# Kernel tuning notes

Measured on AMD Instinct MI355X. Metric: run time of the kernel, lower is better.

The kernel has to match this reference:

```python
import jax, jax.numpy as jnp
import numpy as np
from jax import lax

B, D_IN, LOW_DIM, NUM_CLASS, MOCO_QUEUE = 4096, 1024, 128, 32, 65536
PROTO_M, MOCO_M, EPS = 0.99, 0.999, 1e-12


def l2norm(x, axis=-1):
    n = jnp.linalg.norm(x, axis=axis, keepdims=True)
    return x / jnp.maximum(n, EPS)


def encoder(x, W_cls, b_cls, W_proj):
    # base_encoder returns (class logits, l2-normalized low-dim embedding)
    return x @ W_cls + b_cls, l2norm(x @ W_proj)


def setup_inputs() -> dict:
    key = jax.random.key(0)
    k = jax.random.split(key, 12)
    img_q = jax.random.normal(k[0], (B, D_IN), jnp.float32)
    im_k = jax.random.normal(k[1], (B, D_IN), jnp.float32)
    true_lab = jax.random.randint(k[2], (B,), 0, NUM_CLASS)
    partial_Y = (jax.random.uniform(k[3], (B, NUM_CLASS)) < 0.3).astype(jnp.float32)
    partial_Y = partial_Y.at[jnp.arange(B), true_lab].set(1.0)  # guarantee nonempty candidate set
    W_cls_q = 0.02 * jax.random.normal(k[4], (D_IN, NUM_CLASS), jnp.float32)
    b_cls_q = jnp.zeros((NUM_CLASS,), jnp.float32)
    W_proj_q = 0.02 * jax.random.normal(k[5], (D_IN, LOW_DIM), jnp.float32)
    # key encoder initialized near query encoder (copied then momentum-drifted)
    W_cls_k = W_cls_q + 0.002 * jax.random.normal(k[6], (D_IN, NUM_CLASS), jnp.float32)
    b_cls_k = jnp.zeros((NUM_CLASS,), jnp.float32)
    W_proj_k = W_proj_q + 0.002 * jax.random.normal(k[7], (D_IN, LOW_DIM), jnp.float32)
    queue = jax.random.normal(k[8], (MOCO_QUEUE, LOW_DIM), jnp.float32)
    queue = queue / jnp.maximum(jnp.linalg.norm(queue, axis=0, keepdims=True), EPS)  # F.normalize(queue, dim=0) as in __init__
    queue_pseudo = jax.random.normal(k[9], (MOCO_QUEUE, NUM_CLASS), jnp.float32)
    queue_partial = jax.random.normal(k[10], (MOCO_QUEUE, NUM_CLASS), jnp.float32)
    prototypes = l2norm(jax.random.normal(k[11], (NUM_CLASS, LOW_DIM), jnp.float32))
    return dict(img_q=img_q, im_k=im_k, partial_Y=partial_Y,
                W_cls_q=W_cls_q, b_cls_q=b_cls_q, W_proj_q=W_proj_q,
                W_cls_k=W_cls_k, b_cls_k=b_cls_k, W_proj_k=W_proj_k,
                prototypes=prototypes, queue=queue,
                queue_pseudo=queue_pseudo, queue_partial=queue_partial)


def reference(img_q, im_k, partial_Y, W_cls_q, b_cls_q, W_proj_q,
              W_cls_k, b_cls_k, W_proj_k, prototypes, queue,
              queue_pseudo, queue_partial):
    output, q = encoder(img_q, W_cls_q, b_cls_q, W_proj_q)
    predicted_scores = jax.nn.softmax(output, axis=1) * partial_Y
    pseudo_labels = jnp.argmax(predicted_scores, axis=1)  # (B,) int
    # prototypes are detached before the similarity (clone().detach())
    score_prot = jax.nn.softmax(q @ lax.stop_gradient(prototypes).T, axis=1)
    # order-dependent per-sample EMA scatter (faithful to the python for-loop,
    # including within-batch label collisions) -> lax.scan recurrence
    qd = lax.stop_gradient(q)
    def step(p, xs):
        feat, lab = xs
        return p.at[lab].set(p[lab] * PROTO_M + (1.0 - PROTO_M) * feat), None
    new_protos, _ = lax.scan(step, lax.stop_gradient(prototypes), (qd, pseudo_labels))
    new_protos = l2norm(new_protos)
    # momentum key-encoder update (no grad), then key features
    Wck = lax.stop_gradient(W_cls_k * MOCO_M + W_cls_q * (1.0 - MOCO_M))
    bck = lax.stop_gradient(b_cls_k * MOCO_M + b_cls_q * (1.0 - MOCO_M))
    Wpk = lax.stop_gradient(W_proj_k * MOCO_M + W_proj_q * (1.0 - MOCO_M))
    _, kfeat = encoder(im_k, Wck, bck, Wpk)
    kfeat = lax.stop_gradient(kfeat)
    qv = lax.stop_gradient(queue)
    qp = lax.stop_gradient(queue_pseudo)
    qpt = lax.stop_gradient(queue_partial)
    features = jnp.concatenate([q, kfeat, qv], axis=0)
    pseudo_scores = jnp.concatenate([predicted_scores, predicted_scores, qp], axis=0)
    partial_target = jnp.concatenate([partial_Y, partial_Y, qpt], axis=0)
    # dequeue-and-enqueue at ptr=0 (buffer state update, no grad)
    new_queue = qv.at[0:B].set(kfeat)
    new_queue_pseudo = qp.at[0:B].set(lax.stop_gradient(predicted_scores))
    new_queue_partial = qpt.at[0:B].set(lax.stop_gradient(partial_Y))
    return (output, features, pseudo_scores, partial_target, score_prot,
            new_protos, new_queue, new_queue_pseudo, new_queue_partial)
```

## Files before the change

### kernel.cpp

```cpp
#include <hip/hip_runtime.h>
#include <hip/hip_bf16.h>
#include <stdint.h>


typedef __attribute__((ext_vector_type(8))) short bf16x8;
typedef __attribute__((ext_vector_type(4))) float f32x4;

constexpr size_t O0 = 0;
constexpr size_t O1 = 131072;
constexpr size_t O2 = 9568256;
constexpr size_t O3 = 11927552;
constexpr size_t O4 = 14286848;
constexpr size_t O5 = 14417920;
constexpr size_t O6 = 14422016;
constexpr size_t O7 = 22810624;
constexpr size_t O8 = 24907776;

__device__ __forceinline__ unsigned short f2b(float x) {
  union { float f; uint32_t u; } v; v.f = x;
  uint32_t u = v.u;
  uint32_t r = (u + 0x7fffu + ((u >> 16) & 1u)) >> 16;
  return (unsigned short)r;
}

#define SWZ(r, cb) ((((r) * 128) + (cb)) ^ (((r) & 7) << 4))

__global__ __launch_bounds__(256) void prep(
    const float* __restrict__ Wpq, const float* __restrict__ Wcq,
    const float* __restrict__ Wpk,
    unsigned short* __restrict__ wt_q, unsigned short* __restrict__ wt_pk) {
  const int bid = blockIdx.x;
  const int t = threadIdx.x;
  const float *W1, *W2 = nullptr;
  float a1 = 1.f, a2 = 0.f;
  unsigned short* dst;
  int kb, nbr, nbw, N;
  if (bid < 128) {
    W1 = Wpq; N = 128; kb = (bid & 31) * 32; nbr = nbw = (bid >> 5) * 32;
    dst = wt_q;
  } else if (bid < 160) {
    W1 = Wcq; N = 32; kb = (bid - 128) * 32; nbr = 0; nbw = 128; dst = wt_q;
  } else {
    W1 = Wpk; W2 = Wpq; a1 = 0.999f; a2 = 0.001f; N = 128;
    const int b = bid - 160; kb = (b & 31) * 32; nbr = nbw = (b >> 5) * 32;
    dst = wt_pk;
  }
  __shared__ float tile[32][33];
  const int tx = t & 31, ty = t >> 5;
#pragma unroll
  for (int j = 0; j < 4; ++j) {
    const int k = kb + ty + 8 * j;
    float v = W1[(size_t)k * N + nbr + tx] * a1;
    if (W2) v += W2[(size_t)k * N + nbr + tx] * a2;
    tile[ty + 8 * j][tx] = v;
  }
  __syncthreads();
#pragma unroll
  for (int j = 0; j < 4; ++j) {
    const int n = nbw + ty + 8 * j;
    dst[(size_t)n * 1024 + kb + tx] = f2b(tile[tx][ty + 8 * j]);
  }
}

__global__ __launch_bounds__(320) void gemm_fused(
    const float* __restrict__ img_q, const float* __restrict__ im_k,
    const unsigned short* __restrict__ wt_q,
    const unsigned short* __restrict__ wt_pk,
    const float* __restrict__ bias, const float* __restrict__ partialY,
    const float* __restrict__ protos, float* __restrict__ out,
    int* __restrict__ labels) {
  __shared__ __align__(16) unsigned char smem[28672];
  unsigned char* sA = smem;
  unsigned char* sB = smem + 2048;
  const int bid = blockIdx.x;
  const int t = threadIdx.x;
  const int w = t >> 6, l = t & 63;
  const int ar = l & 15, kg = l >> 4;
  const bool isq = bid < 256;
  const int m0 = (isq ? bid : bid - 256) * 16;
  const float* A = isq ? img_q : im_k;
  const unsigned short* Wt = isq ? wt_q : wt_pk;
  const int BROWS8 = isq ? 1280 : 1024;
  const int arow = t >> 4, acol = t & 15;

  float4 avA, avB;
  uint4 bvA[4], bvB[4];
  if (t < 256) {
    avA = *(const float4*)(A + (size_t)(m0 + arow) * 1024 + acol * 4);
    avB = *(const float4*)(A + (size_t)(m0 + arow) * 1024 + 64 + acol * 4);
  }
#pragma unroll
  for (int i = 0; i < 4; ++i) {
    const int cid = t + i * 320;
    if (cid < BROWS8) {
      const int r = cid >> 3, c = cid & 7;
      bvA[i] = *(const uint4*)(Wt + (size_t)r * 1024 + c * 8);
      bvB[i] = *(const uint4*)(Wt + (size_t)r * 1024 + 64 + c * 8);
    }
  }
  f32x4 acc0 = {0.f, 0.f, 0.f, 0.f}, acc1 = {0.f, 0.f, 0.f, 0.f};

#define STAGE(av, bv)                                                        \
  {                                                                          \
    if (t < 256) {                                                           \
      uint2 pk;                                                              \
      pk.x = (uint32_t)f2b(av.x) | ((uint32_t)f2b(av.y) << 16);              \
      pk.y = (uint32_t)f2b(av.z) | ((uint32_t)f2b(av.w) << 16);              \
      *(uint2*)(sA + SWZ(arow, acol * 8)) = pk;                              \
    }                                                                        \
    _Pragma("unroll") for (int i = 0; i < 4; ++i) {                          \
      const int cid = t + i * 320;                                           \
      if (cid < BROWS8) {                                                    \
        const int r = cid >> 3, c = cid & 7;                                 \
        *(uint4*)(sB + SWZ(r, c * 16)) = bv[i];                              \
      }                                                                      \
    }                                                                        \
  }
#define RELOAD(av, bv, kt)                                                   \
  {                                                                          \
    const int k0 = (kt) * 64;                                                \
    if (t < 256)                                                             \
      av = *(const float4*)(A + (size_t)(m0 + arow) * 1024 + k0 + acol * 4); \
    _Pragma("unroll") for (int i = 0; i < 4; ++i) {                          \
      const int cid = t + i * 320;                                           \
      if (cid < BROWS8) {                                                    \
        const int r = cid >> 3, c = cid & 7;                                 \
        bv[i] = *(const uint4*)(Wt + (size_t)r * 1024 + k0 + c * 8);         \
      }                                                                      \
    }                                                                        \
  }
#define MFMA_PHASE()                                                         \
  if (isq || w < 4) {                                                        \
    _Pragma("unroll") for (int s = 0; s < 2; ++s) {                          \
      const int ch = (s * 4 + kg) * 16;                                      \
      bf16x8 a = *(const bf16x8*)(sA + SWZ(ar, ch));                         \
      const int r0 = w * 32 + ar, r1 = w * 32 + 16 + ar;                     \
      bf16x8 b0 = *(const bf16x8*)(sB + SWZ(r0, ch));                        \
      bf16x8 b1 = *(const bf16x8*)(sB + SWZ(r1, ch));                        \
      acc0 = __builtin_amdgcn_mfma_f32_16x16x32_bf16(a, b0, acc0, 0, 0, 0);  \
      acc1 = __builtin_amdgcn_mfma_f32_16x16x32_bf16(a, b1, acc1, 0, 0, 0);  \
    }                                                                        \
  }

  for (int it = 0; it < 16; it += 2) {
    STAGE(avA, bvA);
    if (it + 2 < 16) RELOAD(avA, bvA, it + 2);
    __syncthreads();
    MFMA_PHASE();
    __syncthreads();
    STAGE(avB, bvB);
    if (it + 3 < 16) RELOAD(avB, bvB, it + 3);
    __syncthreads();
    MFMA_PHASE();
    __syncthreads();
  }

  float* pr = (float*)smem;
  float* Crow = (float*)(smem + 16512);
  if (isq || w < 4) {
#pragma unroll
    for (int j = 0; j < 4; ++j) {
      Crow[(kg * 4 + j) * 164 + w * 32 + ar] = acc0[j];
      Crow[(kg * 4 + j) * 164 + w * 32 + 16 + ar] = acc1[j];
    }
  }
  if (isq) {
    for (int i = t; i < 4096; i += 320)
      pr[(i >> 7) * 129 + (i & 127)] = protos[i];
  }
  __syncthreads();

  if (isq) {
    for (int r = w; r < 16; r += 5) {
      const int grow = m0 + r;
      const float* cr = Crow + r * 164;
      float logit = -1e30f;
      if (l < 32) logit = cr[128 + l] + bias[l];
      float m = logit;
      for (int o = 32; o; o >>= 1) m = fmaxf(m, __shfl_xor(m, o));
      const float e = (l < 32) ? __expf(logit - m) : 0.f;
      float ssum = e;
      for (int o = 32; o; o >>= 1) ssum += __shfl_xor(ssum, o);
      const float py = (l < 32) ? partialY[(size_t)grow * 32 + l] : 0.f;
      const float p = e / ssum * py;
      if (l < 32) {
        out[O0 + (size_t)grow * 32 + l] = logit;
        out[O2 + (size_t)grow * 32 + l] = p;
        out[O2 + (size_t)(4096 + grow) * 32 + l] = p;
        out[O7 + (size_t)grow * 32 + l] = p;
        out[O3 + (size_t)grow * 32 + l] = py;
        out[O3 + (size_t)(4096 + grow) * 32 + l] = py;
        out[O8 + (size_t)grow * 32 + l] = py;
      }
      float av = (l < 32) ? p : -1.f;
      int ai = (l < 32) ? l : 1000;
      for (int o = 32; o; o >>= 1) {
        const float ov = __shfl_xor(av, o);
        const int oi = __shfl_xor(ai, o);
        if (ov > av || (ov == av && oi < ai)) { av = ov; ai = oi; }
      }
      if (l == 0) labels[grow] = ai;
      float v0 = cr[l], v1 = cr[64 + l];
      float ss = v0 * v0 + v1 * v1;
      for (int o = 32; o; o >>= 1) ss += __shfl_xor(ss, o);
      const float den = fmaxf(sqrtf(ss), 1e-12f);
      v0 /= den; v1 /= den;
      out[O1 + (size_t)grow * 128 + l] = v0;
      out[O1 + (size_t)grow * 128 + 64 + l] = v1;
      Crow[r * 164 + l] = v0;
      Crow[r * 164 + 64 + l] = v1;
      const int c = l & 31;
      const int dh = (l >> 5) * 64;
      float acc = 0.f;
#pragma unroll
      for (int d = 0; d < 64; ++d)
        acc += Crow[r * 164 + dh + d] * pr[c * 129 + dh + d];
      acc += __shfl_xor(acc, 32);
      float sm = acc;
      for (int o = 16; o; o >>= 1) sm = fmaxf(sm, __shfl_xor(sm, o));
      const float ee = __expf(acc - sm);
      float s2 = ee;
      for (int o = 16; o; o >>= 1) s2 += __shfl_xor(s2, o);
      if (l < 32) out[O4 + (size_t)grow * 32 + l] = ee / s2;
    }
  } else if (w < 4) {
    for (int r = w; r < 16; r += 4) {
      const int grow = m0 + r;
      const float* cr = Crow + r * 164;
      float v0 = cr[l], v1 = cr[64 + l];
      float ss = v0 * v0 + v1 * v1;
      for (int o = 32; o; o >>= 1) ss += __shfl_xor(ss, o);
      const float den = fmaxf(sqrtf(ss), 1e-12f);
      v0 /= den; v1 /= den;
      out[O1 + (size_t)(4096 + grow) * 128 + l] = v0;
      out[O1 + (size_t)(4096 + grow) * 128 + 64 + l] = v1;
      out[O6 + (size_t)grow * 128 + l] = v0;
      out[O6 + (size_t)grow * 128 + 64 + l] = v1;
    }
  }
}

__global__ __launch_bounds__(256) void tail_all(
    const float* __restrict__ queue, const float* __restrict__ qp,
    const float* __restrict__ qpt, const int* __restrict__ labels,
    const float* __restrict__ protos, float* __restrict__ out) {
  const int bid = blockIdx.x;
  const int t = threadIdx.x;
  if (bid < 32) {
    __shared__ int lab[4096];
    __shared__ int list[4096];
    __shared__ int wtot[4];
    __shared__ float red[2];
    const int c = bid;
    const int w = t >> 6, l = t & 63;
    for (int i = t; i < 4096; i += 256) lab[i] = labels[i];
    __syncthreads();
    int cn = 0;
#pragma unroll
    for (int j = 0; j < 16; ++j) {
      const int jj = (j + t) & 15;
      cn += (lab[t * 16 + jj] == c) ? 1 : 0;
    }
    int inc = cn;
    for (int o = 1; o < 64; o <<= 1) {
      const int n = __shfl_up(inc, o);
      if (l >= o) inc += n;
    }
    if (l == 63) wtot[w] = inc;
    __syncthreads();
    int base = 0;
    for (int ww = 0; ww < w; ++ww) base += wtot[ww];
    const int k = wtot[0] + wtot[1] + wtot[2] + wtot[3];
    int off = base + inc - cn;
    for (int j = 0; j < 16; ++j) {
      const int i = t * 16 + j;
      if (lab[i] == c) list[off++] = i;
    }
    __syncthreads();
    float* wf = (float*)lab;
    for (int j = t; j < k; j += 256)
      wf[j] = 0.01f * __powf(0.99f, (float)(k - 1 - j));
    __syncthreads();
    float acc = 0.f;
    if (t < 128) {
      const float* qfeat = out + O1;
      float a0 = protos[(size_t)c * 128 + t] * __powf(0.99f, (float)k);
      float a1 = 0.f, a2 = 0.f, a3 = 0.f;
      int j = 0;
      for (; j + 4 <= k; j += 4) {
        a0 += wf[j]     * qfeat[(size_t)list[j] * 128 + t];
        a1 += wf[j + 1] * qfeat[(size_t)list[j + 1] * 128 + t];
        a2 += wf[j + 2] * qfeat[(size_t)list[j + 2] * 128 + t];
        a3 += wf[j + 3] * qfeat[(size_t)list[j + 3] * 128 + t];
      }
      for (; j < k; ++j) a0 += wf[j] * qfeat[(size_t)list[j] * 128 + t];
      acc = (a0 + a1) + (a2 + a3);
      float ss = acc * acc;
      for (int o = 32; o; o >>= 1) ss += __shfl_xor(ss, o);
      if ((t & 63) == 0) red[t >> 6] = ss;
    }
    __syncthreads();
    if (t < 128)
      out[O5 + (size_t)c * 128 + t] = acc / fmaxf(sqrtf(red[0] + red[1]), 1e-12f);
  } else {
    constexpr long NQ4 = (long)65536 * 128 / 4;
    constexpr long NP4 = (long)65536 * 32 / 4;
    constexpr long TOT = NQ4 + 2 * NP4;
    float4* o4 = (float4*)out;
    for (long idx = (long)(bid - 32) * 256 + t; idx < TOT; idx += 3072L * 256) {
      if (idx < NQ4) {
        const float4 v = ((const float4*)queue)[idx];
        o4[O1 / 4 + (2L * 4096 * 128) / 4 + idx] = v;
        if ((idx >> 5) >= 4096) o4[O6 / 4 + idx] = v;
      } else if (idx < NQ4 + NP4) {
        const long i = idx - NQ4;
        const float4 v = ((const float4*)qp)[i];
        o4[O2 / 4 + (2L * 4096 * 32) / 4 + i] = v;
        if ((i >> 3) >= 4096) o4[O7 / 4 + i] = v;
      } else {
        const long i = idx - NQ4 - NP4;
        const float4 v = ((const float4*)qpt)[i];
        o4[O3 / 4 + (2L * 4096 * 32) / 4 + i] = v;
        if ((i >> 3) >= 4096) o4[O8 / 4 + i] = v;
      }
    }
  }
}

extern "C" void kernel_launch(void* const* d_in, const int* in_sizes, int n_in,
                              void* d_out, int out_size, void* d_ws, size_t ws_size,
                              hipStream_t stream) {
  const float* img_q    = (const float*)d_in[0];
  const float* im_k     = (const float*)d_in[1];
  const float* partialY = (const float*)d_in[2];
  const float* W_cls_q  = (const float*)d_in[3];
  const float* b_cls_q  = (const float*)d_in[4];
  const float* W_proj_q = (const float*)d_in[5];
  const float* W_proj_k = (const float*)d_in[8];
  const float* protos   = (const float*)d_in[9];
  const float* queue    = (const float*)d_in[10];
  const float* queue_ps = (const float*)d_in[11];
  const float* queue_pt = (const float*)d_in[12];
  float* out = (float*)d_out;

  unsigned short* wt_q  = (unsigned short*)d_ws;
  unsigned short* wt_pk = wt_q + 160 * 1024;
  int* labels = (int*)(wt_pk + 128 * 1024);

  prep<<<288, 256, 0, stream>>>(W_proj_q, W_cls_q, W_proj_k, wt_q, wt_pk);
  gemm_fused<<<512, 320, 0, stream>>>(img_q, im_k, wt_q, wt_pk, b_cls_q,
                                      partialY, protos, out, labels);
  tail_all<<<3104, 256, 0, stream>>>(queue, queue_ps, queue_pt, labels,
                                     protos, out);
}
```

Baseline: 279.9 us.

## Stage full A tile in LDS once and stream B directly from global

The 16-row activation tile is converted to bf16 and written to swizzled LDS in a single upfront pass. The per-k-step double-buffered A and B staging loop with its many barriers is removed. Each wave now reads its 32 weight rows straight from global/L2 into registers for the MFMAs. This trades barrier and LDS-store overhead for uncoalesced per-lane 16-byte global loads of B and less latency hiding across k-steps.

After: 237.8 us. 1.18x faster.

```diff
diff --git a/kernel.cpp b/kernel.cpp
--- a/kernel.cpp
+++ b/kernel.cpp
@@ -22,8 +22,6 @@
   uint32_t r = (u + 0x7fffu + ((u >> 16) & 1u)) >> 16;
   return (unsigned short)r;
 }
-
-#define SWZ(r, cb) ((((r) * 128) + (cb)) ^ (((r) & 7) << 4))
 
 __global__ __launch_bounds__(256) void prep(
     const float* __restrict__ Wpq, const float* __restrict__ Wcq,
@@ -69,9 +67,7 @@
     const float* __restrict__ bias, const float* __restrict__ partialY,
     const float* __restrict__ protos, float* __restrict__ out,
     int* __restrict__ labels) {
-  __shared__ __align__(16) unsigned char smem[28672];
-  unsigned char* sA = smem;
-  unsigned char* sB = smem + 2048;
+  __shared__ __align__(16) unsigned char smem[32768];
   const int bid = blockIdx.x;
   const int t = threadIdx.x;
   const int w = t >> 6, l = t & 63;
@@ -80,84 +76,46 @@
   const int m0 = (isq ? bid : bid - 256) * 16;
   const float* A = isq ? img_q : im_k;
   const unsigned short* Wt = isq ? wt_q : wt_pk;
-  const int BROWS8 = isq ? 1280 : 1024;
-  const int arow = t >> 4, acol = t & 15;
-
-  float4 avA, avB;
-  uint4 bvA[4], bvB[4];
+  const int nstrips = isq ? 5 : 4;
+
   if (t < 256) {
-    avA = *(const float4*)(A + (size_t)(m0 + arow) * 1024 + acol * 4);
-    avB = *(const float4*)(A + (size_t)(m0 + arow) * 1024 + 64 + acol * 4);
-  }
-#pragma unroll
-  for (int i = 0; i < 4; ++i) {
-    const int cid = t + i * 320;
-    if (cid < BROWS8) {
-      const int r = cid >> 3, c = cid & 7;
-      bvA[i] = *(const uint4*)(Wt + (size_t)r * 1024 + c * 8);
-      bvB[i] = *(const uint4*)(Wt + (size_t)r * 1024 + 64 + c * 8);
-    }
-  }
+    const int r = t >> 4, cb = (t & 15) * 4;
+    const float* ap = A + (size_t)(m0 + r) * 1024;
+    const int sw = (r & 7) << 4;
+#pragma unroll
+    for (int j = 0; j < 16; ++j) {
+      const int col = cb + j * 64;
+      const float4 v = *(const float4*)(ap + col);
+      uint2 pk;
+      pk.x = (uint32_t)f2b(v.x) | ((uint32_t)f2b(v.y) << 16);
+      pk.y = (uint32_t)f2b(v.z) | ((uint32_t)f2b(v.w) << 16);
+      *(uint2*)(smem + r * 2048 + ((col * 2) ^ sw)) = pk;
+    }
+  }
+  __syncthreads();
+
   f32x4 acc0 = {0.f, 0.f, 0.f, 0.f}, acc1 = {0.f, 0.f, 0.f, 0.f};
-
-#define STAGE(av, bv)                                                        \
-  {                                                                          \
-    if (t < 256) {                                                           \
-      uint2 pk;                                                              \
-      pk.x = (uint32_t)f2b(av.x) | ((uint32_t)f2b(av.y) << 16);              \
-      pk.y = (uint32_t)f2b(av.z) | ((uint32_t)f2b(av.w) << 16);              \
-      *(uint2*)(sA + SWZ(arow, acol * 8)) = pk;                              \
-    }                                                                        \
-    _Pragma("unroll") for (int i = 0; i < 4; ++i) {                          \
-      const int cid = t + i * 320;                                           \
-      if (cid < BROWS8) {                                                    \
-        const int r = cid >> 3, c = cid & 7;                                 \
-        *(uint4*)(sB + SWZ(r, c * 16)) = bv[i];                              \
-      }                                                                      \
-    }                                                                        \
-  }
-#define RELOAD(av, bv, kt)                                                   \
-  {                                                                          \
-    const int k0 = (kt) * 64;                                                \
-    if (t < 256)                                                             \
-      av = *(const float4*)(A + (size_t)(m0 + arow) * 1024 + k0 + acol * 4); \
-    _Pragma("unroll") for (int i = 0; i < 4; ++i) {                          \
-      const int cid = t + i * 320;                                           \
-      if (cid < BROWS8) {                                                    \
-        const int r = cid >> 3, c = cid & 7;                                 \
-        bv[i] = *(const uint4*)(Wt + (size_t)r * 1024 + k0 + c * 8);         \
-      }                                                                      \
-    }                                                                        \
-  }
-#define MFMA_PHASE()                                                         \
-  if (isq || w < 4) {                                                        \
-    _Pragma("unroll") for (int s = 0; s < 2; ++s) {                          \
-      const int ch = (s * 4 + kg) * 16;                                      \
-      bf16x8 a = *(const bf16x8*)(sA + SWZ(ar, ch));                         \
-      const int r0 = w * 32 + ar, r1 = w * 32 + 16 + ar;                     \
-      bf16x8 b0 = *(const bf16x8*)(sB + SWZ(r0, ch));                        \
-      bf16x8 b1 = *(const bf16x8*)(sB + SWZ(r1, ch));                        \
-      acc0 = __builtin_amdgcn_mfma_f32_16x16x32_bf16(a, b0, acc0, 0, 0, 0);  \
-      acc1 = __builtin_amdgcn_mfma_f32_16x16x32_bf16(a, b1, acc1, 0, 0, 0);  \
-    }                                                                        \
-  }
-
-  for (int it = 0; it < 16; it += 2) {
-    STAGE(avA, bvA);
-    if (it + 2 < 16) RELOAD(avA, bvA, it + 2);
-    __syncthreads();
-    MFMA_PHASE();
-    __syncthreads();
-    STAGE(avB, bvB);
-    if (it + 3 < 16) RELOAD(avB, bvB, it + 3);
-    __syncthreads();
-    MFMA_PHASE();
-    __syncthreads();
-  }
+  if (w < nstrips) {
+    const int cs = w * 32;
+    const unsigned short* b0p = Wt + (size_t)(cs + ar) * 1024;
+    const unsigned short* b1p = Wt + (size_t)(cs + 16 + ar) * 1024;
+    const int abase = ar * 2048;
+    const int asw = (ar & 7) << 4;
+#pragma unroll 4
+    for (int kk = 0; kk < 32; ++kk) {
+      const int k0 = kk * 32 + kg * 8;
+      bf16x8 a = *(const bf16x8*)(smem + abase + ((k0 * 2) ^ asw));
+      bf16x8 b0 = *(const bf16x8*)(b0p + k0);
+      bf16x8 b1 = *(const bf16x8*)(b1p + k0);
+      acc0 = __builtin_amdgcn_mfma_f32_16x16x32_bf16(a, b0, acc0, 0, 0, 0);
+      acc1 = __builtin_amdgcn_mfma_f32_16x16x32_bf16(a, b1, acc1, 0, 0, 0);
+    }
+  }
+  __syncthreads();
 
   float* pr = (float*)smem;
   float* Crow = (float*)(smem + 16512);
-  if (isq || w < 4) {
+  if (w < nstrips) {
 #pragma unroll
     for (int j = 0; j < 4; ++j) {
       Crow[(kg * 4 + j) * 164 + w * 32 + ar] = acc0[j];
```
